# Kernel optimization log

Measured on AMD Instinct MI355X. Metric: run time of the kernel, lower is better.

The kernel has to match this reference:

```python
import jax, jax.numpy as jnp
import numpy as np

VNUM = 50000
OUT = 128
E = 1600000
EPS = 1e-7


def setup_inputs() -> dict:
    key = jax.random.key(0)
    k = jax.random.split(key, 8)
    sidx = jax.random.randint(k[0], (E,), 0, VNUM, dtype=jnp.int64 if jax.config.jax_enable_x64 else jnp.int32)
    tidx = jax.random.randint(k[1], (E,), 0, VNUM, dtype=sidx.dtype)
    enorm = jax.random.uniform(k[2], (E,), dtype=jnp.float32)
    # edge signs +-1 as in signed graph conv
    esgn = jnp.where(jax.random.uniform(k[3], (E,)) < 0.5, -1.0, 1.0).astype(jnp.float32)
    # vrepr initialized trunc_normal(std=0.1) (zero_init=False)
    vrepr = 0.1 * jax.random.truncated_normal(k[4], -2.0, 2.0, (VNUM, OUT), dtype=jnp.float32)
    lim = 1.0 / np.sqrt(OUT)
    loc_w = jax.random.uniform(k[5], (OUT, OUT), jnp.float32, -lim, lim)
    loc_b = jnp.zeros((OUT,), jnp.float32)
    std_w = jax.random.uniform(k[6], (OUT, OUT), jnp.float32, -lim, lim)
    std_b = jnp.zeros((OUT,), jnp.float32)
    return {"sidx": sidx, "tidx": tidx, "enorm": enorm, "esgn": esgn,
            "vrepr": vrepr, "loc_w": loc_w, "loc_b": loc_b,
            "std_w": std_w, "std_b": std_b}


def reference(sidx, tidx, enorm, esgn, vrepr, loc_w, loc_b, std_w, std_b):
    # GraphConv: edge-weighted gather + scatter-add aggregation
    msg = vrepr[sidx] * (esgn * enorm)[:, None]          # [E, OUT]
    ptr = jax.ops.segment_sum(msg, tidx, num_segments=VNUM)  # [VNUM, OUT]
    loc = ptr @ loc_w.T + loc_b                          # Normal loc
    std = jax.nn.softplus(ptr @ std_w.T + std_b) + EPS   # Normal scale
    return loc, std
```

## Files before the change

kernel.cpp:

```cpp
#include <hip/hip_runtime.h>
#include <math.h>

#define VNUM 50000
#define OUTF 128
#define NEDGE 1600000
#define EPSF 1e-7f

#define CONV_BLOCKS 6250
#define BFRAG_BLOCKS 64

#define CHUNK 2048
#define NCB 49
#define COARSE_BLOCKS 782
#define BSTRIDE 36864
#define NSUB 4
#define FINE_BLOCKS (NCB * NSUB)

typedef __attribute__((ext_vector_type(8))) short short8;
typedef __attribute__((ext_vector_type(4))) float v4f;

__device__ __forceinline__ unsigned short f2bf(float f) {
    union { float f; unsigned int u; } c; c.f = f;
    unsigned int u = c.u;
    return (unsigned short)((u + 0x7FFFu + ((u >> 16) & 1u)) >> 16);
}
__device__ __forceinline__ float bf16_lo(unsigned int p) {
    union { unsigned int u; float f; } c; c.u = p << 16; return c.f;
}
__device__ __forceinline__ float bf16_hi(unsigned int p) {
    union { unsigned int u; float f; } c; c.u = p & 0xFFFF0000u; return c.f;
}

__device__ __forceinline__ int wave_incl_scan(int v, int lane) {
#pragma unroll
    for (int off = 1; off < 64; off <<= 1) {
        const int o = __shfl_up(v, off, 64);
        if (lane >= off) v += o;
    }
    return v;
}

__global__ __launch_bounds__(256) void prep_kernel(
    const float* __restrict__ vrepr, unsigned int* __restrict__ vrepr16,
    int* __restrict__ ccursor, int* __restrict__ offs,
    const float* __restrict__ loc_w, const float* __restrict__ std_w,
    unsigned int* bfrag)
{
    const int b = blockIdx.x, tid = threadIdx.x;
    if (b < CONV_BLOCKS) {
        const size_t base = (size_t)b * 1024 + tid * 4;
        const float4 v = *reinterpret_cast<const float4*>(vrepr + base);
        uint2 o;
        o.x = (unsigned)f2bf(v.x) | ((unsigned)f2bf(v.y) << 16);
        o.y = (unsigned)f2bf(v.z) | ((unsigned)f2bf(v.w) << 16);
        *reinterpret_cast<uint2*>(vrepr16 + base / 2) = o;
    } else if (b == CONV_BLOCKS) {
        if (tid < NCB) ccursor[tid] = tid * BSTRIDE;
        if (tid == 63) offs[VNUM] = NEDGE;
    } else {
        const int p = (b - (CONV_BLOCKS + 1)) * 256 + tid;
        const int j2 = p & 3, lq = (p >> 2) & 63, ks = (p >> 8) & 3, ct = p >> 10;
        const int k = ks * 32 + (lq >> 4) * 8 + j2 * 2;
        const int n = ct * 16 + (lq & 15);
        const float* wsrc = (n >> 7) ? std_w : loc_w;
        const int c = n & 127;
        bfrag[p] = (unsigned)f2bf(wsrc[c * 128 + k]) |
                   ((unsigned)f2bf(wsrc[c * 128 + k + 1]) << 16);
    }
}

__global__ __launch_bounds__(256) void coarse_kernel(
    const int* __restrict__ sidx, const int* __restrict__ tidx,
    const float* __restrict__ enorm, const float* __restrict__ esgn,
    int* __restrict__ ccursor, uint2* __restrict__ coarse8)
{
    __shared__ uint2 lrec[CHUNK];
    __shared__ int lcnt[4][NCB];
    __shared__ int lbase[4][NCB];
    __shared__ int loffs[NCB];
    __shared__ int grun[NCB];

    const int tid = threadIdx.x, lane = tid & 63, wv = tid >> 6;
    const int base = blockIdx.x * CHUNK;
    const int n = min(CHUNK, NEDGE - base);

    for (int i = tid; i < 4 * NCB; i += 256) (&lcnt[0][0])[i] = 0;
    __syncthreads();

    uint2 rec[8];
#pragma unroll
    for (int j = 0; j < 8; ++j) {
        const int e = base + j * 256 + tid;
        if (e < NEDGE) {
            const int t = tidx[e];
            const float w = esgn[e] * enorm[e];
            rec[j].x = ((unsigned)sidx[e] << 16) | (unsigned)f2bf(w);
            rec[j].y = (unsigned)t;
            atomicAdd(&lcnt[wv][t >> 10], 1);
        }
    }
    __syncthreads();

    if (tid < 64) {
        int c0 = 0, c1 = 0, c2 = 0, c3 = 0, tot = 0;
        if (lane < NCB) {
            c0 = lcnt[0][lane]; c1 = lcnt[1][lane];
            c2 = lcnt[2][lane]; c3 = lcnt[3][lane];
            tot = c0 + c1 + c2 + c3;
        }
        const int inc = wave_incl_scan(tot, lane);
        const int ex = inc - tot;
        if (lane < NCB) {
            loffs[lane]    = ex;
            lbase[0][lane] = ex;
            lbase[1][lane] = ex + c0;
            lbase[2][lane] = ex + c0 + c1;
            lbase[3][lane] = ex + c0 + c1 + c2;
            grun[lane] = atomicAdd(&ccursor[lane], tot);
        }
    }
    __syncthreads();

#pragma unroll
    for (int j = 0; j < 8; ++j) {
        const int e = base + j * 256 + tid;
        if (e < NEDGE) {
            const int cb = (int)(rec[j].y >> 10);
            const int pos = atomicAdd(&lbase[wv][cb], 1);
            lrec[pos] = rec[j];
        }
    }
    __syncthreads();

    for (int i = tid; i < n; i += 256) {
        const uint2 r = lrec[i];
        const int cb = (int)(r.y >> 10);
        coarse8[grun[cb] + (i - loffs[cb])] = r;
    }
}

__global__ __launch_bounds__(1024) void hist_kernel(
    const uint2* __restrict__ coarse8, const int* __restrict__ ccursor,
    int* __restrict__ hcnt)
{
    __shared__ int cnt[1024];
    const int tid = threadIdx.x;
    const int bin = blockIdx.x >> 2, s = blockIdx.x & 3;
    const int bs = bin * BSTRIDE;
    const int len = ccursor[bin] - bs;
    const int qs = bs + ((len * s) >> 2);
    const int qe = bs + ((len * (s + 1)) >> 2);
    cnt[tid] = 0;
    __syncthreads();
    for (int i = qs + tid; i < qe; i += 1024)
        atomicAdd(&cnt[coarse8[i].y & 1023], 1);
    __syncthreads();
    hcnt[blockIdx.x * 1024 + tid] = cnt[tid];
}

__global__ __launch_bounds__(1024) void scatter_fine_kernel(
    const uint2* __restrict__ coarse8, const int* __restrict__ ccursor,
    const int* __restrict__ hcnt, int* __restrict__ offs,
    unsigned int* __restrict__ pairs)
{
    __shared__ int cur[1024];
    __shared__ int wsum[16];
    __shared__ int sh_s0;
    const int tid = threadIdx.x, lane = tid & 63, wv = tid >> 6;
    const int bin = blockIdx.x >> 2, s = blockIdx.x & 3;
    const int bs = bin * BSTRIDE;

    if (tid < 64) {
        const int lenl = (tid < NCB) ? (ccursor[tid] - tid * BSTRIDE) : 0;
        const int incc = wave_incl_scan(lenl, tid);
        if (tid == bin) sh_s0 = incc - lenl;
    }

    const int len = ccursor[bin] - bs;
    const int qs = bs + ((len * s) >> 2);
    const int qe = bs + ((len * (s + 1)) >> 2);

    const int c0 = hcnt[(bin * 4 + 0) * 1024 + tid];
    const int c1 = hcnt[(bin * 4 + 1) * 1024 + tid];
    const int c2 = hcnt[(bin * 4 + 2) * 1024 + tid];
    const int c3 = hcnt[(bin * 4 + 3) * 1024 + tid];
    const int tot = c0 + c1 + c2 + c3;
    const int pre = (s > 0 ? c0 : 0) + (s > 1 ? c1 : 0) + (s > 2 ? c2 : 0);

    const int inc = wave_incl_scan(tot, lane);
    if (lane == 63) wsum[wv] = inc;
    __syncthreads();
    if (tid == 0) {
        int run = 0;
        for (int i = 0; i < 16; ++i) { const int t = wsum[i]; wsum[i] = run; run += t; }
    }
    __syncthreads();
    const int ex = sh_s0 + wsum[wv] + inc - tot;
    const int gv = (bin << 10) + tid;
    if (s == 0 && gv < VNUM) offs[gv] = ex;
    cur[tid] = ex + pre;
    __syncthreads();

    for (int i = qs + tid; i < qe; i += 1024) {
        const uint2 r = coarse8[i];
        const int pos = atomicAdd(&cur[r.y & 1023], 1);
        pairs[pos] = r.x;
    }
}

__global__ __launch_bounds__(256) void aggregate_kernel(
    const int* __restrict__ offs, const unsigned int* __restrict__ pairs,
    const unsigned int* __restrict__ vrepr16, unsigned int* __restrict__ accu)
{
    const int v = blockIdx.x * 4 + (threadIdx.x >> 6);
    const int l = threadIdx.x & 63;
    int i = offs[v];
    const int end = offs[v + 1];

    float a0 = 0.0f, a1 = 0.0f;
    for (; i + 12 <= end; i += 12) {
        unsigned p[12], r[12];
#pragma unroll
        for (int j = 0; j < 12; ++j) p[j] = pairs[i + j];
#pragma unroll
        for (int j = 0; j < 12; ++j) r[j] = vrepr16[(size_t)(p[j] >> 16) * 64 + l];
#pragma unroll
        for (int j = 0; j < 12; ++j) {
            const float w = bf16_lo(p[j]);
            a0 = fmaf(bf16_lo(r[j]), w, a0);
            a1 = fmaf(bf16_hi(r[j]), w, a1);
        }
    }
    for (; i + 4 <= end; i += 4) {
        unsigned p[4], r[4];
#pragma unroll
        for (int j = 0; j < 4; ++j) p[j] = pairs[i + j];
#pragma unroll
        for (int j = 0; j < 4; ++j) r[j] = vrepr16[(size_t)(p[j] >> 16) * 64 + l];
#pragma unroll
        for (int j = 0; j < 4; ++j) {
            const float w = bf16_lo(p[j]);
            a0 = fmaf(bf16_lo(r[j]), w, a0);
            a1 = fmaf(bf16_hi(r[j]), w, a1);
        }
    }
    for (; i < end; ++i) {
        const unsigned p = pairs[i];
        const unsigned r = vrepr16[(size_t)(p >> 16) * 64 + l];
        const float w = bf16_lo(p);
        a0 = fmaf(bf16_lo(r), w, a0); a1 = fmaf(bf16_hi(r), w, a1);
    }
    const unsigned pk = (unsigned)f2bf(a0) | ((unsigned)f2bf(a1) << 16);
    __builtin_nontemporal_store(pk, accu + (size_t)v * 128 + l);
}

__global__ __launch_bounds__(256) void gemm_mfma_kernel(
    const unsigned int* accu, const unsigned int* __restrict__ bfrag,
    const float* __restrict__ loc_b, const float* __restrict__ std_b,
    float* out)
{
    __shared__ unsigned short tile[16][136];
    const int t = threadIdx.x;
    const int row0 = blockIdx.x * 16;
    const int l = t & 63, w = t >> 6;

    short8 bfr[4][4];
#pragma unroll
    for (int ct = 0; ct < 4; ++ct)
#pragma unroll
        for (int ks = 0; ks < 4; ++ks)
            bfr[ct][ks] = *reinterpret_cast<const short8*>(
                bfrag + ((((w * 4 + ct) * 4 + ks) * 64 + l) << 2));

    {
        const uint4 av = *reinterpret_cast<const uint4*>(
            accu + (size_t)(row0 + (t >> 4)) * 128 + (t & 15) * 4);
        *reinterpret_cast<uint4*>(&tile[t >> 4][(t & 15) * 8]) = av;
    }
    __syncthreads();

    const int m = l & 15, q = l >> 4;
    v4f accv[4];
#pragma unroll
    for (int ct = 0; ct < 4; ++ct) accv[ct] = (v4f){0.0f, 0.0f, 0.0f, 0.0f};

#pragma unroll
    for (int ks = 0; ks < 4; ++ks) {
        const short8 a = *reinterpret_cast<const short8*>(&tile[m][ks * 32 + q * 8]);
#pragma unroll
        for (int ct = 0; ct < 4; ++ct)
            accv[ct] = __builtin_amdgcn_mfma_f32_16x16x32_bf16(
                a, bfr[ct][ks], accv[ct], 0, 0, 0);
    }

#pragma unroll
    for (int ct = 0; ct < 4; ++ct) {
        const int colg = (w * 4 + ct) * 16 + m;
        const int h = colg >> 7, c = colg & 127;
        const float bias = (h ? std_b : loc_b)[c];
        float* dst = out + (h ? (size_t)VNUM * OUTF : (size_t)0);
#pragma unroll
        for (int reg = 0; reg < 4; ++reg) {
            const int row = row0 + q * 4 + reg;
            float x = accv[ct][reg] + bias;
            if (h) x = fmaxf(x, 0.0f) + log1pf(expf(-fabsf(x))) + EPSF;
            dst[(size_t)row * OUTF + c] = x;
        }
    }
}

__global__ __launch_bounds__(256) void gemm_fallback_kernel(
    const unsigned int* accu,
    const float* __restrict__ loc_w, const float* __restrict__ loc_b,
    const float* __restrict__ std_w, const float* __restrict__ std_b,
    float* out)
{
    __shared__ float tile[16][OUTF];
    const int t = threadIdx.x;
    const int row0 = blockIdx.x * 16;
    {
        const uint4 av = *reinterpret_cast<const uint4*>(
            accu + (size_t)(row0 + (t >> 4)) * 128 + (t & 15) * 4);
        float* dst = &tile[t >> 4][(t & 15) * 8];
        dst[0] = bf16_lo(av.x); dst[1] = bf16_hi(av.x);
        dst[2] = bf16_lo(av.y); dst[3] = bf16_hi(av.y);
        dst[4] = bf16_lo(av.z); dst[5] = bf16_hi(av.z);
        dst[6] = bf16_lo(av.w); dst[7] = bf16_hi(av.w);
    }
    __syncthreads();
    const int is_std = t >> 7;
    const int c = t & 127;
    const float* w = (is_std ? std_w : loc_w) + (size_t)c * OUTF;
    const float bias = is_std ? std_b[c] : loc_b[c];
    float accv[16];
#pragma unroll
    for (int r = 0; r < 16; ++r) accv[r] = 0.0f;
    for (int k = 0; k < OUTF; k += 4) {
        const float4 wv = *reinterpret_cast<const float4*>(w + k);
#pragma unroll
        for (int r = 0; r < 16; ++r) {
            const float4 pv = *reinterpret_cast<const float4*>(&tile[r][k]);
            float a = accv[r];
            a = fmaf(pv.x, wv.x, a); a = fmaf(pv.y, wv.y, a);
            a = fmaf(pv.z, wv.z, a); a = fmaf(pv.w, wv.w, a);
            accv[r] = a;
        }
    }
    float* dst_base = out + (is_std ? (size_t)VNUM * OUTF : (size_t)0);
#pragma unroll
    for (int r = 0; r < 16; ++r) {
        const float x = accv[r] + bias;
        dst_base[(size_t)(row0 + r) * OUTF + c] =
            is_std ? (fmaxf(x, 0.0f) + log1pf(expf(-fabsf(x))) + EPSF) : x;
    }
}

extern "C" void kernel_launch(void* const* d_in, const int* in_sizes, int n_in,
                              void* d_out, int out_size, void* d_ws, size_t ws_size,
                              hipStream_t stream) {
    const int*   sidx  = (const int*)  d_in[0];
    const int*   tidx  = (const int*)  d_in[1];
    const float* enorm = (const float*)d_in[2];
    const float* esgn  = (const float*)d_in[3];
    const float* vrepr = (const float*)d_in[4];
    const float* loc_w = (const float*)d_in[5];
    const float* loc_b = (const float*)d_in[6];
    const float* std_w = (const float*)d_in[7];
    const float* std_b = (const float*)d_in[8];

    float* out = (float*)d_out;

    uint2* coarse8 = (uint2*)out;
    unsigned int* accu = (unsigned int*)out;

    unsigned int* sbase   = (unsigned int*)(out + (size_t)VNUM * OUTF);
    unsigned int* pairs   = sbase;
    unsigned int* vrepr16 = sbase + NEDGE;
    int* offs    = (int*)(sbase + NEDGE + (size_t)VNUM * 64);
    int* ccursor = offs + VNUM + 1;
    int* hcnt    = ccursor + NCB;

    const bool use_ws = ws_size >= 16384 * sizeof(unsigned int);
    unsigned int* bfrag = use_ws ? (unsigned int*)d_ws : nullptr;

    const int prep_blocks = CONV_BLOCKS + 1 + (use_ws ? BFRAG_BLOCKS : 0);
    prep_kernel        <<<prep_blocks, 256, 0, stream>>>(vrepr, vrepr16, ccursor,
                                                         offs, loc_w, std_w, bfrag);
    coarse_kernel      <<<COARSE_BLOCKS, 256, 0, stream>>>(sidx, tidx, enorm, esgn,
                                                           ccursor, coarse8);
    hist_kernel        <<<FINE_BLOCKS, 1024, 0, stream>>>(coarse8, ccursor, hcnt);
    scatter_fine_kernel<<<FINE_BLOCKS, 1024, 0, stream>>>(coarse8, ccursor, hcnt,
                                                          offs, pairs);
    aggregate_kernel   <<<VNUM / 4, 256, 0, stream>>>(offs, pairs, vrepr16, accu);

    if (use_ws) {
        gemm_mfma_kernel<<<VNUM / 16, 256, 0, stream>>>(accu, bfrag, loc_b, std_b, out);
    } else {
        gemm_fallback_kernel<<<VNUM / 16, 256, 0, stream>>>(accu, loc_w, loc_b,
                                                            std_w, std_b, out);
    }
}
```

Baseline: 228.3 us.

## Split coarse records into SoA arrays and fuse vrepr conversion into histogram

Coarse-bucketed edge records are now stored as a 32-bit payload array plus a 16-bit target-low array instead of 8-byte structs. The histogram pass reads only the 2-byte field, and the scatter pass reads 6 bytes per record instead of 8. The fp32-to-bf16 conversion of vrepr moves out of the prep kernel into extra blocks of the histogram kernel, so it runs beside the bandwidth-light histogram. The trade-off is two separate global stores per record in the coarse kernel, and 16-bit stores that may coalesce less well.

```diff
diff --git a/kernel.cpp b/kernel.cpp
--- a/kernel.cpp
+++ b/kernel.cpp
@@ -6,7 +6,6 @@
 #define NEDGE 1600000
 #define EPSF 1e-7f
 
-#define CONV_BLOCKS 6250
 #define BFRAG_BLOCKS 64
 
 #define CHUNK 2048
@@ -15,6 +14,7 @@
 #define BSTRIDE 36864
 #define NSUB 4
 #define FINE_BLOCKS (NCB * NSUB)
+#define CONV_BLOCKS 782
 
 typedef __attribute__((ext_vector_type(8))) short short8;
 typedef __attribute__((ext_vector_type(4))) float v4f;
@@ -41,24 +41,16 @@
 }
 
 __global__ __launch_bounds__(256) void prep_kernel(
-    const float* __restrict__ vrepr, unsigned int* __restrict__ vrepr16,
     int* __restrict__ ccursor, int* __restrict__ offs,
     const float* __restrict__ loc_w, const float* __restrict__ std_w,
     unsigned int* bfrag)
 {
     const int b = blockIdx.x, tid = threadIdx.x;
-    if (b < CONV_BLOCKS) {
-        const size_t base = (size_t)b * 1024 + tid * 4;
-        const float4 v = *reinterpret_cast<const float4*>(vrepr + base);
-        uint2 o;
-        o.x = (unsigned)f2bf(v.x) | ((unsigned)f2bf(v.y) << 16);
-        o.y = (unsigned)f2bf(v.z) | ((unsigned)f2bf(v.w) << 16);
-        *reinterpret_cast<uint2*>(vrepr16 + base / 2) = o;
-    } else if (b == CONV_BLOCKS) {
+    if (b == 0) {
         if (tid < NCB) ccursor[tid] = tid * BSTRIDE;
         if (tid == 63) offs[VNUM] = NEDGE;
     } else {
-        const int p = (b - (CONV_BLOCKS + 1)) * 256 + tid;
+        const int p = (b - 1) * 256 + tid;
         const int j2 = p & 3, lq = (p >> 2) & 63, ks = (p >> 8) & 3, ct = p >> 10;
         const int k = ks * 32 + (lq >> 4) * 8 + j2 * 2;
         const int n = ct * 16 + (lq & 15);
@@ -72,9 +64,11 @@
 __global__ __launch_bounds__(256) void coarse_kernel(
     const int* __restrict__ sidx, const int* __restrict__ tidx,
     const float* __restrict__ enorm, const float* __restrict__ esgn,
-    int* __restrict__ ccursor, uint2* __restrict__ coarse8)
-{
-    __shared__ uint2 lrec[CHUNK];
+    int* __restrict__ ccursor,
+    unsigned int* __restrict__ c8m, unsigned short* __restrict__ c8v)
+{
+    __shared__ unsigned int   lrecm[CHUNK];
+    __shared__ unsigned short lrecv[CHUNK];
     __shared__ int lcnt[4][NCB];
     __shared__ int lbase[4][NCB];
     __shared__ int loffs[NCB];
@@ -87,15 +81,16 @@
     for (int i = tid; i < 4 * NCB; i += 256) (&lcnt[0][0])[i] = 0;
     __syncthreads();
 
-    uint2 rec[8];
+    unsigned int rm[8];
+    unsigned short rv[8];
 #pragma unroll
     for (int j = 0; j < 8; ++j) {
         const int e = base + j * 256 + tid;
         if (e < NEDGE) {
             const int t = tidx[e];
             const float w = esgn[e] * enorm[e];
-            rec[j].x = ((unsigned)sidx[e] << 16) | (unsigned)f2bf(w);
-            rec[j].y = (unsigned)t;
+            rm[j] = ((unsigned)sidx[e] << 16) | (unsigned)f2bf(w);
+            rv[j] = (unsigned short)t;
             atomicAdd(&lcnt[wv][t >> 10], 1);
         }
     }
@@ -125,43 +120,62 @@
     for (int j = 0; j < 8; ++j) {
         const int e = base + j * 256 + tid;
         if (e < NEDGE) {
-            const int cb = (int)(rec[j].y >> 10);
+            const int cb = (int)rv[j] >> 10;
             const int pos = atomicAdd(&lbase[wv][cb], 1);
-            lrec[pos] = rec[j];
+            lrecm[pos] = rm[j];
+            lrecv[pos] = rv[j];
         }
     }
     __syncthreads();
 
     for (int i = tid; i < n; i += 256) {
-        const uint2 r = lrec[i];
-        const int cb = (int)(r.y >> 10);
-        coarse8[grun[cb] + (i - loffs[cb])] = r;
-    }
-}
-
-__global__ __launch_bounds__(1024) void hist_kernel(
-    const uint2* __restrict__ coarse8, const int* __restrict__ ccursor,
-    int* __restrict__ hcnt)
+        const unsigned int   m = lrecm[i];
+        const unsigned short v = lrecv[i];
+        const int cb = (int)v >> 10;
+        const int dst = grun[cb] + (i - loffs[cb]);
+        c8m[dst] = m;
+        c8v[dst] = v;
+    }
+}
+
+__global__ __launch_bounds__(1024) void hist_conv_kernel(
+    const unsigned short* __restrict__ c8v, const int* __restrict__ ccursor,
+    int* __restrict__ hcnt,
+    const float* __restrict__ vrepr, unsigned int* __restrict__ vrepr16)
 {
     __shared__ int cnt[1024];
-    const int tid = threadIdx.x;
-    const int bin = blockIdx.x >> 2, s = blockIdx.x & 3;
-    const int bs = bin * BSTRIDE;
-    const int len = ccursor[bin] - bs;
-    const int qs = bs + ((len * s) >> 2);
-    const int qe = bs + ((len * (s + 1)) >> 2);
-    cnt[tid] = 0;
-    __syncthreads();
-    for (int i = qs + tid; i < qe; i += 1024)
-        atomicAdd(&cnt[coarse8[i].y & 1023], 1);
-    __syncthreads();
-    hcnt[blockIdx.x * 1024 + tid] = cnt[tid];
+    const int b = blockIdx.x, tid = threadIdx.x;
+    if (b < FINE_BLOCKS) {
+        const int bin = b >> 2, s = b & 3;
+        const int bs = bin * BSTRIDE;
+        const int len = ccursor[bin] - bs;
+        const int qs = bs + ((len * s) >> 2);
+        const int qe = bs + ((len * (s + 1)) >> 2);
+        cnt[tid] = 0;
+        __syncthreads();
+        for (int i = qs + tid; i < qe; i += 1024)
+            atomicAdd(&cnt[c8v[i] & 1023], 1);
+        __syncthreads();
+        hcnt[b * 1024 + tid] = cnt[tid];
+    } else {
+        const int gid = (b - FINE_BLOCKS) * 1024 + tid;
+        if (gid < (VNUM * OUTF) / 8) {
+            const float4 v0 = *reinterpret_cast<const float4*>(vrepr + (size_t)gid * 8);
+            const float4 v1 = *reinterpret_cast<const float4*>(vrepr + (size_t)gid * 8 + 4);
+            uint4 pk;
+            pk.x = (unsigned)f2bf(v0.x) | ((unsigned)f2bf(v0.y) << 16);
+            pk.y = (unsigned)f2bf(v0.z) | ((unsigned)f2bf(v0.w) << 16);
+            pk.z = (unsigned)f2bf(v1.x) | ((unsigned)f2bf(v1.y) << 16);
+            pk.w = (unsigned)f2bf(v1.z) | ((unsigned)f2bf(v1.w) << 16);
+            *reinterpret_cast<uint4*>(vrepr16 + (size_t)gid * 4) = pk;
+        }
+    }
 }
 
 __global__ __launch_bounds__(1024) void scatter_fine_kernel(
-    const uint2* __restrict__ coarse8, const int* __restrict__ ccursor,
-    const int* __restrict__ hcnt, int* __restrict__ offs,
-    unsigned int* __restrict__ pairs)
+    const unsigned int* __restrict__ c8m, const unsigned short* __restrict__ c8v,
+    const int* __restrict__ ccursor, const int* __restrict__ hcnt,
+    int* __restrict__ offs, unsigned int* __restrict__ pairs)
 {
     __shared__ int cur[1024];
     __shared__ int wsum[16];
@@ -202,9 +216,9 @@
     __syncthreads();
 
     for (int i = qs + tid; i < qe; i += 1024) {
-        const uint2 r = coarse8[i];
-        const int pos = atomicAdd(&cur[r.y & 1023], 1);
-        pairs[pos] = r.x;
+        const unsigned short v = c8v[i];
+        const int pos = atomicAdd(&cur[(int)v & 1023], 1);
+        pairs[pos] = c8m[i];
     }
 }
 
@@ -370,8 +384,9 @@
 
     float* out = (float*)d_out;
 
-    uint2* coarse8 = (uint2*)out;
-    unsigned int* accu = (unsigned int*)out;
+    unsigned int*   c8m  = (unsigned int*)out;
+    unsigned short* c8v  = (unsigned short*)(c8m + (size_t)NCB * BSTRIDE);
+    unsigned int*   accu = (unsigned int*)out;
 
     unsigned int* sbase   = (unsigned int*)(out + (size_t)VNUM * OUTF);
     unsigned int* pairs   = sbase;
@@ -383,13 +398,14 @@
     const bool use_ws = ws_size >= 16384 * sizeof(unsigned int);
     unsigned int* bfrag = use_ws ? (unsigned int*)d_ws : nullptr;
 
-    const int prep_blocks = CONV_BLOCKS + 1 + (use_ws ? BFRAG_BLOCKS : 0);
-    prep_kernel        <<<prep_blocks, 256, 0, stream>>>(vrepr, vrepr16, ccursor,
-                                                         offs, loc_w, std_w, bfrag);
+    const int prep_blocks = 1 + (use_ws ? BFRAG_BLOCKS : 0);
+    prep_kernel        <<<prep_blocks, 256, 0, stream>>>(ccursor, offs,
+                                                         loc_w, std_w, bfrag);
     coarse_kernel      <<<COARSE_BLOCKS, 256, 0, stream>>>(sidx, tidx, enorm, esgn,
-                                                           ccursor, coarse8);
-    hist_kernel        <<<FINE_BLOCKS, 1024, 0, stream>>>(coarse8, ccursor, hcnt);
-    scatter_fine_kernel<<<FINE_BLOCKS, 1024, 0, stream>>>(coarse8, ccursor, hcnt,
+                                                           ccursor, c8m, c8v);
+    hist_conv_kernel   <<<FINE_BLOCKS + CONV_BLOCKS, 1024, 0, stream>>>(
+                            c8v, ccursor, hcnt, vrepr, vrepr16);
+    scatter_fine_kernel<<<FINE_BLOCKS, 1024, 0, stream>>>(c8m, c8v, ccursor, hcnt,
                                                           offs, pairs);
     aggregate_kernel   <<<VNUM / 4, 256, 0, stream>>>(offs, pairs, vrepr16, accu);
 
```

Measured after the change: 225.5 us (median of 2 runs). Within noise of the previous version (-1.2%).
